# Performance work log

Hardware: AMD Instinct MI355X
Metric: run time of the kernel (lower is better)

## Reference

```python
import jax, jax.numpy as jnp
import numpy as np

IN, HID, OUT = 512, 2048, 128
B, T = 8, 512


def setup_inputs() -> dict:
    key = jax.random.key(0)
    ks = jax.random.split(key, 8)
    k = 1.0 / np.sqrt(HID)  # torch default init scale for RNN/Linear
    u = lambda kk, shape: jax.random.uniform(kk, shape, jnp.float32, -k, k)
    return {
        "x": jax.random.normal(ks[0], (B, T, IN), jnp.float32),
        "W_ih": u(ks[1], (HID, IN)),
        "b_ih": u(ks[2], (HID,)),
        "W_hh": u(ks[3], (HID, HID)),
        "b_hh": u(ks[4], (HID,)),
        "W_out": u(ks[5], (OUT, HID)),
        "b_out": u(ks[6], (OUT,)),
    }


def reference(x, W_ih, b_ih, W_hh, b_hh, W_out, b_out):
    # Pre-project inputs for all timesteps in one big GEMM: [B,T,HID]
    xp = jnp.einsum("bti,hi->bth", x, W_ih) + b_ih + b_hh

    def step(h, xt):  # h: [B,HID], xt: [B,HID]
        h = jnp.tanh(xt + h @ W_hh.T)
        return h, h

    h0 = jnp.zeros((x.shape[0], W_hh.shape[0]), x.dtype)
    _, hs = jax.lax.scan(step, h0, jnp.swapaxes(xp, 0, 1))  # hs: [T,B,HID]
    hs = jnp.swapaxes(hs, 0, 1)  # [B,T,HID]
    return hs @ W_out.T + b_out  # [B,T,OUT]
```

## Files before the change

kernel.cpp:

```cpp
#include <hip/hip_runtime.h>


#define IN_K   512
#define HID    2048
#define OUTN   128
#define BB     8
#define TSTEPS 512
#define NWG    32
#define JPW    64
#define SENT   0xFF80FF80u

typedef __bf16 bf16x8 __attribute__((ext_vector_type(8)));
typedef unsigned short u16x8 __attribute__((ext_vector_type(8)));
typedef unsigned int u32x4 __attribute__((ext_vector_type(4)));
typedef float f32v4 __attribute__((ext_vector_type(4)));

union Frag8 { u16x8 u; bf16x8 b; u32x4 d; };

__device__ __forceinline__ unsigned short f2bf(float f) {
  unsigned int u = __float_as_uint(f);
  return (unsigned short)((u + 0x7FFFu + ((u >> 16) & 1u)) >> 16);
}

__device__ __forceinline__ float tanh_fast(float x) {
  return 1.0f - 2.0f / (__expf(2.0f * x) + 1.0f);
}

__global__ __launch_bounds__(256)
void sentinel_kernel(u32x4* __restrict__ p) {
  const size_t i = (size_t)blockIdx.x * 256 + threadIdx.x;
  u32x4 v; v[0] = SENT; v[1] = SENT; v[2] = SENT; v[3] = SENT;
  p[i] = v;
}

template<int EPI>
__global__ __launch_bounds__(256, 2)
void gemm_kernel(const void* __restrict__ Aptr, const float* __restrict__ Bptr,
                 const float* __restrict__ bias0, const float* __restrict__ bias1,
                 float* __restrict__ Cout, const int Kdim, const int Ndim)
{
  __shared__ __align__(16) unsigned short As[64][56];
  __shared__ __align__(16) unsigned short Bs[64][56];

  const int m0 = blockIdx.x * 64;
  const int n0 = blockIdx.y * 64;
  const int tid = threadIdx.x;
  const int w = tid >> 6, l = tid & 63;
  const int l15 = l & 15, lk = (l >> 4) * 8;
  const int wm = (w >> 1) * 32, wn = (w & 1) * 32;

  f32v4 acc[2][2];
  #pragma unroll
  for (int mt = 0; mt < 2; ++mt)
    #pragma unroll
    for (int nt = 0; nt < 2; ++nt)
      #pragma unroll
      for (int r = 0; r < 4; ++r) acc[mt][nt][r] = 0.0f;

  for (int k0 = 0; k0 < Kdim; k0 += 32) {
    __syncthreads();
    if (EPI == 0) {
      const float* A = (const float*)Aptr;
      const int r = tid >> 3, c4 = (tid & 7) * 4;
      #pragma unroll
      for (int it = 0; it < 2; ++it) {
        const float4 v = *(const float4*)(A + (size_t)(m0 + r + it * 32) * Kdim + k0 + c4);
        unsigned short* d = &As[r + it * 32][c4];
        d[0] = f2bf(v.x); d[1] = f2bf(v.y); d[2] = f2bf(v.z); d[3] = f2bf(v.w);
      }
    } else {
      const unsigned short* A = (const unsigned short*)Aptr;
      const int r = tid >> 2, c8 = (tid & 3) * 8;
      const u16x8 v = *(const u16x8*)(A + (size_t)(m0 + r) * Kdim + k0 + c8);
      *(u16x8*)&As[r][c8] = v;
    }
    {
      const int r = tid >> 3, c4 = (tid & 7) * 4;
      #pragma unroll
      for (int it = 0; it < 2; ++it) {
        const float4 v = *(const float4*)(Bptr + (size_t)(n0 + r + it * 32) * Kdim + k0 + c4);
        unsigned short* d = &Bs[r + it * 32][c4];
        d[0] = f2bf(v.x); d[1] = f2bf(v.y); d[2] = f2bf(v.z); d[3] = f2bf(v.w);
      }
    }
    __syncthreads();

    Frag8 af[2], bg[2];
    #pragma unroll
    for (int mt = 0; mt < 2; ++mt) af[mt].u = *(const u16x8*)&As[wm + mt * 16 + l15][lk];
    #pragma unroll
    for (int nt = 0; nt < 2; ++nt) bg[nt].u = *(const u16x8*)&Bs[wn + nt * 16 + l15][lk];
    #pragma unroll
    for (int mt = 0; mt < 2; ++mt)
      #pragma unroll
      for (int nt = 0; nt < 2; ++nt)
        acc[mt][nt] = __builtin_amdgcn_mfma_f32_16x16x32_bf16(af[mt].b, bg[nt].b, acc[mt][nt], 0, 0, 0);
  }

  #pragma unroll
  for (int mt = 0; mt < 2; ++mt)
    #pragma unroll
    for (int nt = 0; nt < 2; ++nt)
      #pragma unroll
      for (int r = 0; r < 4; ++r) {
        const int m = m0 + wm + mt * 16 + (l >> 4) * 4 + r;
        const int n = n0 + wn + nt * 16 + l15;
        float v = acc[mt][nt][r];
        if (EPI == 0) {
          v += bias0[n] + bias1[n];
          const int b = m >> 9, t = m & 511;
          Cout[((size_t)t * BB + b) * Ndim + n] = v;
        } else {
          v += bias0[n];
          Cout[(size_t)m * Ndim + n] = v;
        }
      }
}

__global__ __launch_bounds__(512, 2)
void scan_kernel(const float* __restrict__ Whh, const float* __restrict__ xp,
                 unsigned short* __restrict__ hs)
{
  const int g = blockIdx.x;
  const int tid = threadIdx.x;
  const int w = tid >> 6, l = tid & 63;
  const int l15 = l & 15, lk = (l >> 4) * 8;
  const int jbase = g * JPW;

  Frag8 Bw[4][8];
  #pragma unroll
  for (int jt = 0; jt < 4; ++jt) {
    const int j = jbase + jt * 16 + l15;
    #pragma unroll
    for (int kc = 0; kc < 8; ++kc) {
      const int k = w * 256 + kc * 32 + lk;
      const float4* p = (const float4*)(Whh + (size_t)j * HID + k);
      const float4 u0 = p[0], u1 = p[1];
      Frag8 f;
      f.u[0] = f2bf(u0.x); f.u[1] = f2bf(u0.y); f.u[2] = f2bf(u0.z); f.u[3] = f2bf(u0.w);
      f.u[4] = f2bf(u1.x); f.u[5] = f2bf(u1.y); f.u[6] = f2bf(u1.z); f.u[7] = f2bf(u1.w);
      Bw[jt][kc] = f;
    }
  }

  __shared__ float red[8][4][16][16];
  const int om = tid >> 5;
  const int oj2 = (tid & 31) * 2;
  const int jt_e = oj2 >> 4, col = oj2 & 15;
  const int arow = l15 & 7;

  for (int t = 0; t < TSTEPS; ++t) {
    float xv0 = 0.f, xv1 = 0.f;
    if (tid < 256) {
      const float2 xv = *(const float2*)(xp + ((size_t)t * BB + om) * HID + jbase + oj2);
      xv0 = xv.x; xv1 = xv.y;
    }

    f32v4 acc[4];
    #pragma unroll
    for (int jt = 0; jt < 4; ++jt)
      #pragma unroll
      for (int r = 0; r < 4; ++r) acc[jt][r] = 0.f;

    if (t > 0) {
      const unsigned short* hb = hs + ((size_t)arow * TSTEPS + (t - 1)) * HID + w * 256 + lk;
      Frag8 a[8];
      unsigned int valid = 0;
      do {
        #pragma unroll
        for (int kc = 0; kc < 8; ++kc) {
          if (!(valid & (1u << kc))) {
            asm volatile("global_load_dwordx4 %0, %1, off offset:%2 sc0 sc1"
                         : "=v"(a[kc].d) : "v"(hb), "n"(kc * 64));
          }
        }
        asm volatile("s_waitcnt vmcnt(0)" ::: "memory");
        __builtin_amdgcn_sched_barrier(0);
        #pragma unroll
        for (int kc = 0; kc < 8; ++kc) {
          if (!(valid & (1u << kc))) {
            unsigned int mv = min(min(a[kc].d[0] ^ SENT, a[kc].d[1] ^ SENT),
                                  min(a[kc].d[2] ^ SENT, a[kc].d[3] ^ SENT));
            if (__all(mv != 0u)) {
              valid |= (1u << kc);
              #pragma unroll
              for (int jt = 0; jt < 4; ++jt)
                acc[jt] = __builtin_amdgcn_mfma_f32_16x16x32_bf16(a[kc].b, Bw[jt][kc].b, acc[jt], 0, 0, 0);
            }
          }
        }
      } while (valid != 0xFFu);
    }

    #pragma unroll
    for (int jt = 0; jt < 4; ++jt)
      #pragma unroll
      for (int r = 0; r < 4; ++r)
        red[w][jt][(l >> 4) * 4 + r][l15] = acc[jt][r];
    __syncthreads();

    if (tid < 256) {
      float s0 = xv0, s1 = xv1;
      #pragma unroll
      for (int wv = 0; wv < 8; ++wv) {
        s0 += red[wv][jt_e][om][col];
        s1 += red[wv][jt_e][om][col + 1];
      }
      const float h0 = tanh_fast(s0), h1 = tanh_fast(s1);
      const unsigned int packed = (unsigned int)f2bf(h0) | ((unsigned int)f2bf(h1) << 16);
      unsigned int* hp = (unsigned int*)(hs + ((size_t)om * TSTEPS + t) * HID + jbase + oj2);
      __hip_atomic_store(hp, packed, __ATOMIC_RELAXED, __HIP_MEMORY_SCOPE_AGENT);
    }
    __syncthreads();
  }
}

extern "C" void kernel_launch(void* const* d_in, const int* in_sizes, int n_in,
                              void* d_out, int out_size, void* d_ws, size_t ws_size,
                              hipStream_t stream)
{
  (void)in_sizes; (void)n_in; (void)out_size; (void)ws_size;
  const float* x    = (const float*)d_in[0];
  const float* Wih  = (const float*)d_in[1];
  const float* bih  = (const float*)d_in[2];
  const float* Whh  = (const float*)d_in[3];
  const float* bhh  = (const float*)d_in[4];
  const float* Wout = (const float*)d_in[5];
  const float* bout = (const float*)d_in[6];
  float* out = (float*)d_out;

  char* ws = (char*)d_ws;
  float* xp          = (float*)(ws);
  unsigned short* hs = (unsigned short*)(ws + (size_t)(32 << 20));

  sentinel_kernel<<<dim3(4096), 256, 0, stream>>>((u32x4*)hs);
  gemm_kernel<0><<<dim3(64, 32), 256, 0, stream>>>(x, Wih, bih, bhh, xp, IN_K, HID);
  scan_kernel<<<dim3(NWG), 512, 0, stream>>>(Whh, xp, hs);
  gemm_kernel<1><<<dim3(64, 2), 256, 0, stream>>>(hs, Wout, bout, nullptr, out, HID, OUTN);
}
```

Before: 1.819 ms.

## Reorder hidden-state layout to time-major and widen scan epilogue stores

Changes the hs buffer layout from [B,T,HID] to [T,B,HID] so each step's hidden state is contiguous, and updates the output GEMM indexing to match. The scan epilogue moves from 256 threads doing 4-byte atomic stores to 64 threads each doing one 16-byte store with sc0 sc1. The xp loads become 32-byte asm loads issued early. The polling loop now waits on the first four h loads before the last four so MFMAs can start sooner. The reduction scratch gets a padded row to avoid LDS bank conflicts. The aim is to cut the per-step global store and load latency on the serial critical path. The risk is torn 16-byte writes being seen by pollers, which the per-fragment sentinel check is meant to catch.

```diff
diff --git a/kernel.cpp b/kernel.cpp
--- a/kernel.cpp
+++ b/kernel.cpp
@@ -112,7 +112,8 @@
           Cout[((size_t)t * BB + b) * Ndim + n] = v;
         } else {
           v += bias0[n];
-          Cout[(size_t)m * Ndim + n] = v;
+          const int b = m & 7, t = m >> 3;
+          Cout[((size_t)b * TSTEPS + t) * Ndim + n] = v;
         }
       }
 }
@@ -143,17 +144,31 @@
     }
   }
 
-  __shared__ float red[8][4][16][16];
-  const int om = tid >> 5;
-  const int oj2 = (tid & 31) * 2;
-  const int jt_e = oj2 >> 4, col = oj2 & 15;
+  __shared__ float red[8][4][16][17];
   const int arow = l15 & 7;
+  const int eb = (tid & 63) >> 3;
+  const int eq = tid & 7;
+  const int ejt = eq >> 1;
+  const int ecol = (eq & 1) * 8;
+
+#define CHECK_MFMA(kc) do {                                                    \
+    unsigned int mv = min(min(a[kc].d[0] ^ SENT, a[kc].d[1] ^ SENT),           \
+                          min(a[kc].d[2] ^ SENT, a[kc].d[3] ^ SENT));          \
+    if (__all(mv != 0u)) {                                                     \
+      valid |= (1u << (kc));                                                   \
+      _Pragma("unroll") for (int jt = 0; jt < 4; ++jt)                         \
+        acc[jt] = __builtin_amdgcn_mfma_f32_16x16x32_bf16(a[kc].b,             \
+                      Bw[jt][(kc)].b, acc[jt], 0, 0, 0);                       \
+    }                                                                          \
+  } while (0)
 
   for (int t = 0; t < TSTEPS; ++t) {
-    float xv0 = 0.f, xv1 = 0.f;
-    if (tid < 256) {
-      const float2 xv = *(const float2*)(xp + ((size_t)t * BB + om) * HID + jbase + oj2);
-      xv0 = xv.x; xv1 = xv.y;
+    u32x4 xr0, xr1;
+    if (tid < 64) {
+      const float* xq = xp + ((size_t)t * BB + eb) * HID + jbase + eq * 8;
+      asm volatile("global_load_dwordx4 %0, %2, off\n\t"
+                   "global_load_dwordx4 %1, %2, off offset:16"
+                   : "=v"(xr0), "=v"(xr1) : "v"(xq));
     }
 
     f32v4 acc[4];
@@ -163,33 +178,33 @@
       for (int r = 0; r < 4; ++r) acc[jt][r] = 0.f;
 
     if (t > 0) {
-      const unsigned short* hb = hs + ((size_t)arow * TSTEPS + (t - 1)) * HID + w * 256 + lk;
+      const unsigned short* hb = hs + ((size_t)(t - 1) * BB + arow) * HID + w * 256 + lk;
       Frag8 a[8];
       unsigned int valid = 0;
-      do {
+      #pragma unroll
+      for (int kc = 0; kc < 8; ++kc)
+        asm volatile("global_load_dwordx4 %0, %1, off offset:%2 sc0 sc1"
+                     : "=v"(a[kc].d) : "v"(hb), "n"(kc * 64));
+      asm volatile("s_waitcnt vmcnt(4)" ::: "memory");
+      __builtin_amdgcn_sched_barrier(0);
+      #pragma unroll
+      for (int kc = 0; kc < 4; ++kc) CHECK_MFMA(kc);
+      asm volatile("s_waitcnt vmcnt(0)" ::: "memory");
+      __builtin_amdgcn_sched_barrier(0);
+      #pragma unroll
+      for (int kc = 4; kc < 8; ++kc) CHECK_MFMA(kc);
+      while (valid != 0xFFu) {
         #pragma unroll
-        for (int kc = 0; kc < 8; ++kc) {
-          if (!(valid & (1u << kc))) {
+        for (int kc = 0; kc < 8; ++kc)
+          if (!(valid & (1u << kc)))
             asm volatile("global_load_dwordx4 %0, %1, off offset:%2 sc0 sc1"
                          : "=v"(a[kc].d) : "v"(hb), "n"(kc * 64));
-          }
-        }
         asm volatile("s_waitcnt vmcnt(0)" ::: "memory");
         __builtin_amdgcn_sched_barrier(0);
         #pragma unroll
-        for (int kc = 0; kc < 8; ++kc) {
-          if (!(valid & (1u << kc))) {
-            unsigned int mv = min(min(a[kc].d[0] ^ SENT, a[kc].d[1] ^ SENT),
-                                  min(a[kc].d[2] ^ SENT, a[kc].d[3] ^ SENT));
-            if (__all(mv != 0u)) {
-              valid |= (1u << kc);
-              #pragma unroll
-              for (int jt = 0; jt < 4; ++jt)
-                acc[jt] = __builtin_amdgcn_mfma_f32_16x16x32_bf16(a[kc].b, Bw[jt][kc].b, acc[jt], 0, 0, 0);
-            }
-          }
-        }
-      } while (valid != 0xFFu);
+        for (int kc = 0; kc < 8; ++kc)
+          if (!(valid & (1u << kc))) CHECK_MFMA(kc);
+      }
     }
 
     #pragma unroll
@@ -199,20 +214,32 @@
         red[w][jt][(l >> 4) * 4 + r][l15] = acc[jt][r];
     __syncthreads();
 
-    if (tid < 256) {
-      float s0 = xv0, s1 = xv1;
-      #pragma unroll
-      for (int wv = 0; wv < 8; ++wv) {
-        s0 += red[wv][jt_e][om][col];
-        s1 += red[wv][jt_e][om][col + 1];
-      }
-      const float h0 = tanh_fast(s0), h1 = tanh_fast(s1);
-      const unsigned int packed = (unsigned int)f2bf(h0) | ((unsigned int)f2bf(h1) << 16);
-      unsigned int* hp = (unsigned int*)(hs + ((size_t)om * TSTEPS + t) * HID + jbase + oj2);
-      __hip_atomic_store(hp, packed, __ATOMIC_RELAXED, __HIP_MEMORY_SCOPE_AGENT);
+    if (tid < 64) {
+      asm volatile("s_waitcnt vmcnt(0)" ::: "memory");
+      __builtin_amdgcn_sched_barrier(0);
+      float xv[8];
+      xv[0] = __uint_as_float(xr0[0]); xv[1] = __uint_as_float(xr0[1]);
+      xv[2] = __uint_as_float(xr0[2]); xv[3] = __uint_as_float(xr0[3]);
+      xv[4] = __uint_as_float(xr1[0]); xv[5] = __uint_as_float(xr1[1]);
+      xv[6] = __uint_as_float(xr1[2]); xv[7] = __uint_as_float(xr1[3]);
+      u32x4 pk;
+      #pragma unroll
+      for (int i2 = 0; i2 < 4; ++i2) {
+        float s0 = xv[i2 * 2], s1 = xv[i2 * 2 + 1];
+        #pragma unroll
+        for (int wv = 0; wv < 8; ++wv) {
+          s0 += red[wv][ejt][eb][ecol + i2 * 2];
+          s1 += red[wv][ejt][eb][ecol + i2 * 2 + 1];
+        }
+        pk[i2] = (unsigned int)f2bf(tanh_fast(s0))
+               | ((unsigned int)f2bf(tanh_fast(s1)) << 16);
+      }
+      unsigned short* hp = hs + ((size_t)t * BB + eb) * HID + jbase + eq * 8;
+      asm volatile("global_store_dwordx4 %0, %1, off sc0 sc1" :: "v"(hp), "v"(pk) : "memory");
     }
     __syncthreads();
   }
+#undef CHECK_MFMA
 }
 
 extern "C" void kernel_launch(void* const* d_in, const int* in_sizes, int n_in,
```

After: 1.925 ms. +5.8%, slower.
